# Performance work log

Measured on AMD Instinct MI355X. Metric: run time of the kernel, lower is better.

The kernel has to match this reference:

```python
import jax, jax.numpy as jnp
import numpy as np

B, T, V, E, U = 8192, 1, 4000, 256, 256
IN = E + E  # GRU input dim: concat(features[B,1,256], embedded tokens[B,1,256]) -> 512


def setup_inputs() -> dict:
    key = jax.random.key(0)
    ks = jax.random.split(key, 8)
    s = 0.05
    return {
        "tokens": jax.random.randint(ks[0], (B, T), 0, V),
        "features": jax.random.normal(ks[1], (B, E), jnp.float32),
        "hidden": jnp.zeros((B, U), jnp.float32),  # unused by the original call (gru gets no initial_state)
        "emb": jax.random.normal(ks[2], (V, E), jnp.float32) * s,
        "gru_kernel": jax.random.normal(ks[3], (IN, 3 * U), jnp.float32) * s,
        "gru_rkernel": jax.random.normal(ks[4], (U, 3 * U), jnp.float32) * s,
        "gru_bias": jnp.zeros((2, 3 * U), jnp.float32),  # reset_after=True: separate input/recurrent biases
        "fc1_w": jax.random.normal(ks[5], (U, U), jnp.float32) * s,
        "fc1_b": jnp.zeros((U,), jnp.float32),
        "fc2_w": jax.random.normal(ks[6], (U, V), jnp.float32) * s,
        "fc2_b": jnp.zeros((V,), jnp.float32),
    }


def reference(tokens, features, hidden, emb, gru_kernel, gru_rkernel, gru_bias,
              fc1_w, fc1_b, fc2_w, fc2_b):
    # Embedding lookup: [B,T,E]
    x = emb[tokens]
    # concat context vector on feature axis (forces T==1): [B,1,E+E]
    x = jnp.concatenate([features[:, None, :], x], axis=-1)
    # Keras GRU called without initial_state -> zeros initial state.
    h0 = jnp.zeros((x.shape[0], U), x.dtype)

    def step(h, xt):  # xt: [B, IN]; Keras GRU v3 (reset_after=True) cell; dropout off at inference
        gx = xt @ gru_kernel + gru_bias[0]      # [B, 3U]
        gh = h @ gru_rkernel + gru_bias[1]      # [B, 3U]
        xz, xr, xn = jnp.split(gx, 3, axis=-1)
        hz, hr, hn = jnp.split(gh, 3, axis=-1)
        z = jax.nn.sigmoid(xz + hz)
        r = jax.nn.sigmoid(xr + hr)
        n = jnp.tanh(xn + r * hn)
        h_new = z * h + (1.0 - z) * n
        return h_new, h_new

    state, seq = jax.lax.scan(step, h0, jnp.swapaxes(x, 0, 1))  # seq: [T,B,U]
    out = jnp.swapaxes(seq, 0, 1)               # [B,T,U]
    y = out @ fc1_w + fc1_b                     # [B,T,U]
    y = y.reshape(-1, y.shape[-1])              # [B*T, U]
    logits = y @ fc2_w + fc2_b                  # [B*T, V]
    return (logits, state)
```

## Files before the change

### kernel.cpp

```cpp
#include <hip/hip_runtime.h>
#include <stdint.h>

typedef unsigned short u16;
typedef __attribute__((ext_vector_type(8))) short bf16x8;
typedef __attribute__((ext_vector_type(4))) float f32x4;

#define Bsz   8192
#define Vv    4000
#define Vpad  4096
#define Ee    256
#define Uu    256
#define INd   512
#define G3    768

__device__ __forceinline__ u16 f2bf(float f) {
    union { float f; uint32_t i; } v; v.f = f;
    uint32_t x = v.i;
    return (u16)((x + 0x7fffu + ((x >> 16) & 1u)) >> 16);
}

__device__ __forceinline__ void gload16(const u16* g, u16* l) {
    __builtin_amdgcn_global_load_lds(
        (const __attribute__((address_space(1))) unsigned int*)g,
        (__attribute__((address_space(3))) unsigned int*)l, 16, 0, 0);
}

__global__ __launch_bounds__(256) void prep_all(
    const float* __restrict__ w1,  u16* __restrict__ w1t,
    const float* __restrict__ fc1, u16* __restrict__ fc1c,
    const float* __restrict__ fc2, u16* __restrict__ fc2t,
    const float* __restrict__ fc1b, const float* __restrict__ fc2b,
    float* __restrict__ bfused)
{
    __shared__ float t[32][33];
    int b = blockIdx.x;
    if (b >= 1472) {
        int nl = (b - 1472) * 256 + threadIdx.x;
        if (nl < Vv) {
            float s = fc2b[nl];
            for (int k = 0; k < Uu; k++)
                s += fc1b[k] * fc2[(size_t)k * Vv + nl];
            bfused[nl] = s;
        }
        return;
    }
    if (b >= 384 && b < 448) {
        int i = (b - 384) * 1024 + threadIdx.x * 4;
        float4 v = *(const float4*)(fc1 + i);
        __align__(8) u16 o[4] = {f2bf(v.x), f2bf(v.y), f2bf(v.z), f2bf(v.w)};
        *(uint2*)&fc1c[i] = *(const uint2*)o;
        return;
    }
    const float* in; u16* out; int K, N, bx, by;
    if (b < 384) { in = w1;  out = w1t;  K = 512; N = 768; bx = b % 24;  by = b / 24; }
    else { b -= 448; in = fc2; out = fc2t; K = 256; N = Vv; bx = b % 128; by = b / 128; }
    int n0 = bx * 32, k0 = by * 32;
    int c = threadIdx.x & 31, r = threadIdx.x >> 5;
    int n = n0 + c;
    #pragma unroll
    for (int i = 0; i < 32; i += 8)
        t[r + i][c] = (n < N) ? in[(size_t)(k0 + r + i) * N + n] : 0.f;
    __syncthreads();
    #pragma unroll
    for (int i = 0; i < 32; i += 8)
        out[(size_t)(n0 + r + i) * K + k0 + c] = f2bf(t[c][r + i]);
}

__global__ __launch_bounds__(256) void gru_fused(
    const int* __restrict__ tokens, const float* __restrict__ features,
    const float* __restrict__ emb,  const u16* __restrict__ BT,
    const float* __restrict__ gb,
    u16* __restrict__ h,
    float* __restrict__ state)
{
    __shared__ __align__(16) u16 As[2][64 * 32];
    __shared__ __align__(16) u16 Bs[2][3][64 * 32];
    __shared__ int tok[64];

    int tid = threadIdx.x;
    int id  = blockIdx.y * gridDim.x + blockIdx.x;
    int sid = (id & 7) * 64 + (id >> 3);
    int m0  = (sid >> 2) * 64;
    int n0  = (sid & 3) * 64;
    if (tid < 64) tok[tid] = tokens[m0 + tid];

    int wid = tid >> 6, lane = tid & 63, quad = lane >> 4, l16 = lane & 15;
    int wm = wid * 16;

    f32x4 acc[3][4] = {};

    int r  = tid >> 2;
    int kc = (tid & 3) * 8;
    const u16* bg = BT + (size_t)(n0 + r) * INd + kc;
    const float* fsrc = features + (size_t)(m0 + r) * Ee + kc;

    #pragma unroll
    for (int g = 0; g < 3; g++)
        gload16(bg + (size_t)g * 256 * INd, &Bs[0][g][tid * 8]);
    float4 a = *(const float4*)fsrc;
    float4 c = *(const float4*)(fsrc + 4);
    {
        u16 o[8] = {f2bf(a.x), f2bf(a.y), f2bf(a.z), f2bf(a.w),
                    f2bf(c.x), f2bf(c.y), f2bf(c.z), f2bf(c.w)};
        *(uint4*)&As[0][tid * 8] = *(const uint4*)o;
    }
    a = *(const float4*)(fsrc + 32);
    c = *(const float4*)(fsrc + 36);

    int cur = 0;
    for (int k0 = 0; k0 < INd; k0 += 32) {
        __syncthreads();
        int k1 = k0 + 32;
        if (k1 < INd) {
            #pragma unroll
            for (int g = 0; g < 3; g++)
                gload16(bg + (size_t)g * 256 * INd + k1, &Bs[cur ^ 1][g][tid * 8]);
            u16 o[8] = {f2bf(a.x), f2bf(a.y), f2bf(a.z), f2bf(a.w),
                        f2bf(c.x), f2bf(c.y), f2bf(c.z), f2bf(c.w)};
            *(uint4*)&As[cur ^ 1][tid * 8] = *(const uint4*)o;
            int k2 = k0 + 64;
            if (k2 < INd) {
                const float* src = (k2 < Ee) ? (fsrc + k2)
                                 : (emb + (size_t)tok[r] * Ee + (k2 - Ee) + kc);
                a = *(const float4*)src;
                c = *(const float4*)(src + 4);
            }
        }
        bf16x8 af = *(const bf16x8*)&As[cur][(wm + l16) * 32 + quad * 8];
        #pragma unroll
        for (int g = 0; g < 3; g++)
            #pragma unroll
            for (int j = 0; j < 4; j++) {
                bf16x8 bfv = *(const bf16x8*)&Bs[cur][g][(j * 16 + l16) * 32 + quad * 8];
                acc[g][j] = __builtin_amdgcn_mfma_f32_16x16x32_bf16(af, bfv, acc[g][j], 0, 0, 0);
            }
        cur ^= 1;
    }

    #pragma unroll
    for (int j = 0; j < 4; j++) {
        int jj = n0 + j * 16 + l16;
        float bz  = gb[jj]          + gb[G3 + jj];
        float br  = gb[Uu + jj]     + gb[G3 + Uu + jj];
        float b0n = gb[2 * Uu + jj];
        float b1n = gb[G3 + 2 * Uu + jj];
        #pragma unroll
        for (int rr = 0; rr < 4; rr++) {
            int b = m0 + wm + quad * 4 + rr;
            float z  = 1.f / (1.f + __expf(-(acc[0][j][rr] + bz)));
            float rg = 1.f / (1.f + __expf(-(acc[1][j][rr] + br)));
            float n  = tanhf(acc[2][j][rr] + b0n + rg * b1n);
            float hv = (1.f - z) * n;
            h[(size_t)b * Uu + jj] = f2bf(hv);
            state[(size_t)b * Uu + jj] = hv;
        }
    }
}

template<int BMt, int BNt, bool OUT_BF16, bool SWZ, bool HAS_BIAS>
__global__ __launch_bounds__(256) void gemm_bt(
    const u16* __restrict__ A, const u16* __restrict__ BT,
    const float* __restrict__ bias, void* __restrict__ Cout,
    int N, int K)
{
    constexpr int NW_N  = (BNt == 128) ? 2 : 1;
    constexpr int NW_M  = 4 / NW_N;
    constexpr int WROWS = BMt / NW_M;
    constexpr int MI    = WROWS / 16;

    __shared__ __align__(16) u16 As[BMt * 32];
    __shared__ __align__(16) u16 Bs[BNt * 32];

    int tid = threadIdx.x;
    int bx  = blockIdx.x, by = blockIdx.y;
    if (SWZ) {
        int nx  = gridDim.x;
        int nwg = nx * gridDim.y;
        int id  = by * nx + bx;
        int sid = (id & 7) * (nwg >> 3) + (id >> 3);
        bx = sid % nx; by = sid / nx;
    }
    int m0   = by * BMt;
    int n0   = bx * BNt;
    int wid  = tid >> 6, lane = tid & 63, quad = lane >> 4, l16 = lane & 15;
    int wm   = (wid / NW_N) * WROWS;
    int wn   = (wid % NW_N) * 64;

    f32x4 acc[MI][4] = {};

    const u16* ag = A  + (size_t)(m0 + (tid >> 2)) * K + (tid & 3) * 8;
    const u16* bg = BT + (size_t)(n0 + (tid >> 2)) * K + (tid & 3) * 8;
    u16* lA = &As[tid * 8];
    u16* lB = &Bs[tid * 8];

    for (int k0 = 0; k0 < K; k0 += 32) {
        __syncthreads();
        #pragma unroll
        for (int s = 0; s < BMt / 64; s++)
            gload16(ag + (size_t)s * 64 * K + k0, lA + s * 64 * 32);
        #pragma unroll
        for (int s = 0; s < BNt / 64; s++)
            gload16(bg + (size_t)s * 64 * K + k0, lB + s * 64 * 32);
        __syncthreads();

        bf16x8 af[MI], bf[4];
        #pragma unroll
        for (int i = 0; i < MI; i++)
            af[i] = *(const bf16x8*)&As[(wm + i * 16 + l16) * 32 + quad * 8];
        #pragma unroll
        for (int j = 0; j < 4; j++)
            bf[j] = *(const bf16x8*)&Bs[(wn + j * 16 + l16) * 32 + quad * 8];
        #pragma unroll
        for (int i = 0; i < MI; i++)
            #pragma unroll
            for (int j = 0; j < 4; j++)
                acc[i][j] = __builtin_amdgcn_mfma_f32_16x16x32_bf16(af[i], bf[j], acc[i][j], 0, 0, 0);
    }

    #pragma unroll
    for (int i = 0; i < MI; i++)
    #pragma unroll
    for (int j = 0; j < 4; j++) {
        int gn = n0 + wn + j * 16 + l16;
        if (gn >= N) continue;
        float bv = HAS_BIAS ? bias[gn] : 0.f;
        #pragma unroll
        for (int r = 0; r < 4; r++) {
            int gm = m0 + wm + i * 16 + quad * 4 + r;
            float v = acc[i][j][r] + bv;
            if (OUT_BF16) ((u16*)Cout)[(size_t)gm * N + gn] = f2bf(v);
            else          ((float*)Cout)[(size_t)gm * N + gn] = v;
        }
    }
}

extern "C" void kernel_launch(void* const* d_in, const int* in_sizes, int n_in,
                              void* d_out, int out_size, void* d_ws, size_t ws_size,
                              hipStream_t stream)
{
    const int*   tokens   = (const int*)d_in[0];
    const float* features = (const float*)d_in[1];
    const float* emb      = (const float*)d_in[3];
    const float* w1       = (const float*)d_in[4];
    const float* gbias    = (const float*)d_in[6];
    const float* fc1w     = (const float*)d_in[7];
    const float* fc1b     = (const float*)d_in[8];
    const float* fc2w     = (const float*)d_in[9];
    const float* fc2b     = (const float*)d_in[10];

    float* logits = (float*)d_out;
    float* state  = logits + (size_t)Bsz * Vv;

    char* ws = (char*)d_ws;
    u16*   w1t    = (u16*)(ws);
    u16*   fc1c   = (u16*)(ws +   786432);
    u16*   fc2t   = (u16*)(ws +   917504);
    u16*   Wt     = (u16*)(ws +  3014656);
    u16*   h      = (u16*)(ws +  5111808);
    float* bfused = (float*)(ws + 9306112);

    prep_all<<<dim3(1488), 256, 0, stream>>>(w1, w1t, fc1w, fc1c, fc2w, fc2t,
                                             fc1b, fc2b, bfused);

    gemm_bt<64, 64, true, false, false><<<dim3(Uu / 64, Vpad / 64), 256, 0, stream>>>(
        fc2t, fc1c, nullptr, (void*)Wt, Uu, Uu);

    gru_fused<<<dim3(Uu / 64, Bsz / 64), 256, 0, stream>>>(
        tokens, features, emb, w1t, gbias, h, state);

    gemm_bt<128, 128, false, true, true><<<dim3(Vpad / 128, Bsz / 128), 256, 0, stream>>>(
        h, Wt, bfused, (void*)logits, Vv, Uu);
}
```

Before: 236.2 us.

## Double-buffer GEMM LDS tiles, drop block swizzle, parallelize fused-bias reduction

The GEMM kernel now double-buffers its LDS A/B tiles: it prefetches the next K-slice with global_load_lds while computing on the current one, which removes one barrier per iteration and overlaps loads with MFMA work. The block-index swizzle used for the large logits GEMM is removed in favour of plain grid mapping. The fused-bias computation in prep_all splits the 256-length dot product across four wavefronts and combines them with an LDS reduction, using more blocks so each serial loop is shorter. The swizzle removal may hurt L2 reuse, and the double buffer depends on the single barrier ordering async LDS loads correctly.

```diff
diff --git a/kernel.cpp b/kernel.cpp
--- a/kernel.cpp
+++ b/kernel.cpp
@@ -33,15 +33,24 @@
     float* __restrict__ bfused)
 {
     __shared__ float t[32][33];
+    __shared__ float red[4][64];
     int b = blockIdx.x;
     if (b >= 1472) {
-        int nl = (b - 1472) * 256 + threadIdx.x;
+        int nl = (b - 1472) * 64 + (threadIdx.x & 63);
+        int kq = threadIdx.x >> 6;
+        float s = 0.f;
         if (nl < Vv) {
-            float s = fc2b[nl];
-            for (int k = 0; k < Uu; k++)
-                s += fc1b[k] * fc2[(size_t)k * Vv + nl];
-            bfused[nl] = s;
-        }
+            #pragma unroll 8
+            for (int k = 0; k < 64; k++) {
+                int kk = kq * 64 + k;
+                s += fc1b[kk] * fc2[(size_t)kk * Vv + nl];
+            }
+        }
+        red[kq][threadIdx.x & 63] = s;
+        __syncthreads();
+        if (kq == 0 && nl < Vv)
+            bfused[nl] = red[0][nl & 63] + red[1][nl & 63] + red[2][nl & 63]
+                       + red[3][nl & 63] + fc2b[nl];
         return;
     }
     if (b >= 384 && b < 448) {
@@ -157,7 +166,7 @@
     }
 }
 
-template<int BMt, int BNt, bool OUT_BF16, bool SWZ, bool HAS_BIAS>
+template<int BMt, int BNt, bool OUT_BF16, bool HAS_BIAS>
 __global__ __launch_bounds__(256) void gemm_bt(
     const u16* __restrict__ A, const u16* __restrict__ BT,
     const float* __restrict__ bias, void* __restrict__ Cout,
@@ -168,20 +177,12 @@
     constexpr int WROWS = BMt / NW_M;
     constexpr int MI    = WROWS / 16;
 
-    __shared__ __align__(16) u16 As[BMt * 32];
-    __shared__ __align__(16) u16 Bs[BNt * 32];
+    __shared__ __align__(16) u16 As[2][BMt * 32];
+    __shared__ __align__(16) u16 Bs[2][BNt * 32];
 
     int tid = threadIdx.x;
-    int bx  = blockIdx.x, by = blockIdx.y;
-    if (SWZ) {
-        int nx  = gridDim.x;
-        int nwg = nx * gridDim.y;
-        int id  = by * nx + bx;
-        int sid = (id & 7) * (nwg >> 3) + (id >> 3);
-        bx = sid % nx; by = sid / nx;
-    }
-    int m0   = by * BMt;
-    int n0   = bx * BNt;
+    int m0   = blockIdx.y * BMt;
+    int n0   = blockIdx.x * BNt;
     int wid  = tid >> 6, lane = tid & 63, quad = lane >> 4, l16 = lane & 15;
     int wm   = (wid / NW_N) * WROWS;
     int wn   = (wid % NW_N) * 64;
@@ -190,31 +191,40 @@
 
     const u16* ag = A  + (size_t)(m0 + (tid >> 2)) * K + (tid & 3) * 8;
     const u16* bg = BT + (size_t)(n0 + (tid >> 2)) * K + (tid & 3) * 8;
-    u16* lA = &As[tid * 8];
-    u16* lB = &Bs[tid * 8];
-
+
+    #pragma unroll
+    for (int s = 0; s < BMt / 64; s++)
+        gload16(ag + (size_t)s * 64 * K, &As[0][tid * 8 + s * 64 * 32]);
+    #pragma unroll
+    for (int s = 0; s < BNt / 64; s++)
+        gload16(bg + (size_t)s * 64 * K, &Bs[0][tid * 8 + s * 64 * 32]);
+
+    int cur = 0;
     for (int k0 = 0; k0 < K; k0 += 32) {
         __syncthreads();
-        #pragma unroll
-        for (int s = 0; s < BMt / 64; s++)
-            gload16(ag + (size_t)s * 64 * K + k0, lA + s * 64 * 32);
-        #pragma unroll
-        for (int s = 0; s < BNt / 64; s++)
-            gload16(bg + (size_t)s * 64 * K + k0, lB + s * 64 * 32);
-        __syncthreads();
+        int k1 = k0 + 32;
+        if (k1 < K) {
+            #pragma unroll
+            for (int s = 0; s < BMt / 64; s++)
+                gload16(ag + (size_t)s * 64 * K + k1, &As[cur ^ 1][tid * 8 + s * 64 * 32]);
+            #pragma unroll
+            for (int s = 0; s < BNt / 64; s++)
+                gload16(bg + (size_t)s * 64 * K + k1, &Bs[cur ^ 1][tid * 8 + s * 64 * 32]);
+        }
 
         bf16x8 af[MI], bf[4];
         #pragma unroll
         for (int i = 0; i < MI; i++)
-            af[i] = *(const bf16x8*)&As[(wm + i * 16 + l16) * 32 + quad * 8];
+            af[i] = *(const bf16x8*)&As[cur][(wm + i * 16 + l16) * 32 + quad * 8];
         #pragma unroll
         for (int j = 0; j < 4; j++)
-            bf[j] = *(const bf16x8*)&Bs[(wn + j * 16 + l16) * 32 + quad * 8];
+            bf[j] = *(const bf16x8*)&Bs[cur][(wn + j * 16 + l16) * 32 + quad * 8];
         #pragma unroll
         for (int i = 0; i < MI; i++)
             #pragma unroll
             for (int j = 0; j < 4; j++)
                 acc[i][j] = __builtin_amdgcn_mfma_f32_16x16x32_bf16(af[i], bf[j], acc[i][j], 0, 0, 0);
+        cur ^= 1;
     }
 
     #pragma unroll
@@ -259,15 +269,15 @@
     u16*   h      = (u16*)(ws +  5111808);
     float* bfused = (float*)(ws + 9306112);
 
-    prep_all<<<dim3(1488), 256, 0, stream>>>(w1, w1t, fc1w, fc1c, fc2w, fc2t,
+    prep_all<<<dim3(1536), 256, 0, stream>>>(w1, w1t, fc1w, fc1c, fc2w, fc2t,
                                              fc1b, fc2b, bfused);
 
-    gemm_bt<64, 64, true, false, false><<<dim3(Uu / 64, Vpad / 64), 256, 0, stream>>>(
+    gemm_bt<64, 64, true, false><<<dim3(Uu / 64, Vpad / 64), 256, 0, stream>>>(
         fc2t, fc1c, nullptr, (void*)Wt, Uu, Uu);
 
     gru_fused<<<dim3(Uu / 64, Bsz / 64), 256, 0, stream>>>(
         tokens, features, emb, w1t, gbias, h, state);
 
-    gemm_bt<128, 128, false, true, true><<<dim3(Vpad / 128, Bsz / 128), 256, 0, stream>>>(
+    gemm_bt<128, 128, false, true><<<dim3(Vpad / 128, Bsz / 128), 256, 0, stream>>>(
         h, Wt, bfused, (void*)logits, Vv, Uu);
 }
```

Result: faster. 220.0 us (-6.9%).
